# Kernel tuning notes

Measured on AMD Instinct MI355X. Metric: run time of the kernel, lower is better.

The kernel has to match this reference:

```python
import jax, jax.numpy as jnp
import numpy as np

D_MODEL = 1024
N_LAYER = 4
VOCAB = 50288  # 50277 padded to multiple of 16
D_STATE = 128
D_CONV = 4
HEADDIM = 64
CHUNK = 64
D_INNER = 2 * D_MODEL            # expand=2 -> 2048
NHEADS = D_INNER // HEADDIM      # 32
D_IN_PROJ = 2 * D_INNER + 2 * D_STATE + NHEADS  # ngroups=1
CONV_DIM = D_INNER + 2 * D_STATE
BATCH = 1
SEQLEN = 1024
EPS = 1e-5


def silu(x):
    return x * jax.nn.sigmoid(x)


def rmsnorm(x, w, z=None):
    if z is not None:
        x = x * silu(z)
    return x * jax.lax.rsqrt(jnp.mean(x * x, axis=-1, keepdims=True) + EPS) * w


def segsum(x):
    # x: (..., T) -> (..., T, T) with segment sums below diagonal, -inf above
    T = x.shape[-1]
    xe = jnp.broadcast_to(x[..., None], x.shape + (T,))
    mask_lo = jnp.tril(jnp.ones((T, T), dtype=bool), -1)
    xe = jnp.where(mask_lo, xe, 0.0)
    s = jnp.cumsum(xe, axis=-2)
    mask = jnp.tril(jnp.ones((T, T), dtype=bool), 0)
    return jnp.where(mask, s, -jnp.inf)


def ssd(x, dt, A, B, C, Dp):
    # x: (b,s,h,p), dt/A-broadcast: (b,s,h), B/C: (b,s,n) (ngroups=1), Dp: (h,)
    b, s = x.shape[0], x.shape[1]
    nchunks = s // CHUNK
    xD = x * Dp[:, None]
    Adt = A * dt                      # (b,s,h)
    xdt = x * dt[..., None]
    xr = xdt.reshape(b, nchunks, CHUNK, NHEADS, HEADDIM)
    Ar = Adt.reshape(b, nchunks, CHUNK, NHEADS).transpose(0, 3, 1, 2)  # (b,h,c,l)
    Br = B.reshape(b, nchunks, CHUNK, D_STATE)
    Cr = C.reshape(b, nchunks, CHUNK, D_STATE)
    A_cumsum = jnp.cumsum(Ar, axis=-1)                  # (b,h,c,l)
    L = jnp.exp(segsum(Ar))                             # (b,h,c,l,l)
    Y_diag = jnp.einsum('bcln,bcsn,bhcls,bcshp->bclhp', Cr, Br, L, xr)
    decay_states = jnp.exp(A_cumsum[..., -1:] - A_cumsum)
    states = jnp.einsum('bcln,bhcl,bclhp->bchpn', Br, decay_states, xr)
    states = jnp.concatenate([jnp.zeros_like(states[:, :1]), states], axis=1)
    decay_chunk = jnp.exp(segsum(jnp.pad(A_cumsum[..., -1], ((0, 0), (0, 0), (1, 0)))))
    new_states = jnp.einsum('bhzc,bchpn->bzhpn', decay_chunk, states)
    states = new_states[:, :-1]
    state_decay_out = jnp.exp(A_cumsum)
    Y_off = jnp.einsum('bcln,bchpn,bhcl->bclhp', Cr, states, state_decay_out)
    Y = (Y_diag + Y_off).reshape(b, s, NHEADS, HEADDIM) + xD
    return Y


def mamba2_forward(input_ids, embedding, norm_w, in_proj_w, conv_w, conv_b,
                   dt_bias, A_log, D, mixer_norm_w, out_proj_w, norm_f_w):
    h = embedding[input_ids]  # (b,s,d_model)
    for l in range(N_LAYER):
        u = rmsnorm(h, norm_w[l])
        zxbcdt = u @ in_proj_w[l].T  # (b,s,d_in_proj)
        z = zxbcdt[..., :D_INNER]
        xBC = zxbcdt[..., D_INNER:D_INNER + CONV_DIM]
        dt = jax.nn.softplus(zxbcdt[..., -NHEADS:] + dt_bias[l])
        # causal depthwise conv1d
        xc = jnp.transpose(xBC, (0, 2, 1))
        xc = jax.lax.conv_general_dilated(
            xc, conv_w[l], (1,), [(D_CONV - 1, 0)],
            dimension_numbers=('NCH', 'OIH', 'NCH'),
            feature_group_count=CONV_DIM) + conv_b[l][None, :, None]
        xBC = silu(jnp.transpose(xc, (0, 2, 1)))
        x = xBC[..., :D_INNER].reshape(BATCH, SEQLEN, NHEADS, HEADDIM)
        B = xBC[..., D_INNER:D_INNER + D_STATE]
        C = xBC[..., D_INNER + D_STATE:]
        A = -jnp.exp(A_log[l])  # (h,)
        y = ssd(x, dt, A, B, C, D[l])
        y = rmsnorm(y.reshape(BATCH, SEQLEN, D_INNER), mixer_norm_w[l], z)
        h = h + y @ out_proj_w[l].T
    h = rmsnorm(h, norm_f_w)
    return h @ embedding.T  # tied lm_head


def setup_inputs() -> dict:
    key = jax.random.key(0)
    ks = jax.random.split(key, 10)
    def rn(k, shape, s=0.02):
        return jax.random.normal(k, shape, jnp.float32) * s
    return {
        'input_ids': jax.random.randint(ks[0], (BATCH, SEQLEN), 0, VOCAB, jnp.int32),
        'embedding': rn(ks[1], (VOCAB, D_MODEL)),
        'norm_w': jnp.ones((N_LAYER, D_MODEL), jnp.float32),
        'in_proj_w': rn(ks[2], (N_LAYER, D_IN_PROJ, D_MODEL)),
        'conv_w': rn(ks[3], (N_LAYER, CONV_DIM, 1, D_CONV), 0.2),
        'conv_b': jnp.zeros((N_LAYER, CONV_DIM), jnp.float32),
        'dt_bias': rn(ks[4], (N_LAYER, NHEADS), 0.5),
        'A_log': jnp.log(jax.random.uniform(ks[5], (N_LAYER, NHEADS), jnp.float32, 1.0, 16.0)),
        'D': jnp.ones((N_LAYER, NHEADS), jnp.float32) + rn(ks[6], (N_LAYER, NHEADS), 0.1),
        'mixer_norm_w': jnp.ones((N_LAYER, D_INNER), jnp.float32),
        'out_proj_w': rn(ks[7], (N_LAYER, D_MODEL, D_INNER)),
        'norm_f_w': jnp.ones((D_MODEL,), jnp.float32),
    }


def reference(input_ids, embedding, norm_w, in_proj_w, conv_w, conv_b,
              dt_bias, A_log, D, mixer_norm_w, out_proj_w, norm_f_w):
    return mamba2_forward(input_ids, embedding, norm_w, in_proj_w, conv_w, conv_b,
                          dt_bias, A_log, D, mixer_norm_w, out_proj_w, norm_f_w)
```

## Files before the change

kernel.cpp:

```cpp
#include <hip/hip_runtime.h>
#include <hip/hip_bf16.h>
#include <math.h>

#define D_MODEL   1024
#define VOCAB     50288
#define D_STATE   128
#define D_CONV    4
#define HEADDIM   64
#define CHUNK     64
#define D_INNER   2048
#define NHEADS    32
#define D_IN_PROJ 4384
#define CONV_DIM  2304
#define SEQ       1024
#define NCHUNKS   16
#define EPS       1e-5f
#define SZH       1048576

typedef __bf16 bf16x8 __attribute__((ext_vector_type(8)));
typedef __bf16 bf16x4 __attribute__((ext_vector_type(4)));
typedef float  f32x4  __attribute__((ext_vector_type(4)));

__device__ __forceinline__ float blockReduceSum256(float v, float* sm) {
    #pragma unroll
    for (int off = 32; off > 0; off >>= 1) v += __shfl_down(v, off);
    if ((threadIdx.x & 63) == 0) sm[threadIdx.x >> 6] = v;
    __syncthreads();
    return sm[0] + sm[1] + sm[2] + sm[3];
}

__device__ __forceinline__ float sigmoidf_(float x) { return 1.0f / (1.0f + expf(-x)); }

__device__ __forceinline__ void gload_lds16(const __bf16* g, __bf16* l) {
    __builtin_amdgcn_global_load_lds(
        (const __attribute__((address_space(1))) void*)g,
        (__attribute__((address_space(3))) void*)l,
        16, 0, 0);
}

__global__ void cvt_bf16_k(const float* __restrict__ src, __bf16* __restrict__ dst, long n) {
    long i = ((long)blockIdx.x * 256 + threadIdx.x) * 8;
    long stride = (long)gridDim.x * 256 * 8;
    for (; i < n; i += stride) {
        float4 a = *(const float4*)(src + i);
        float4 b = *(const float4*)(src + i + 4);
        bf16x8 o;
        o[0] = (__bf16)a.x; o[1] = (__bf16)a.y; o[2] = (__bf16)a.z; o[3] = (__bf16)a.w;
        o[4] = (__bf16)b.x; o[5] = (__bf16)b.y; o[6] = (__bf16)b.z; o[7] = (__bf16)b.w;
        *(bf16x8*)(dst + i) = o;
    }
}

__global__ void gather_k(const int* __restrict__ ids, const float* __restrict__ emb,
                         float* __restrict__ h) {
    int s = blockIdx.x;
    int id = ids[s];
    const float4* src = (const float4*)(emb + (size_t)id * D_MODEL);
    float4* dst = (float4*)(h + (size_t)s * D_MODEL);
    dst[threadIdx.x] = src[threadIdx.x];
}

__global__ void rmsnorm_k(const float* __restrict__ x, const float* __restrict__ w,
                          float* __restrict__ o) {
    __shared__ float red[4];
    int s = blockIdx.x, t = threadIdx.x;
    float4 v = ((const float4*)(x + (size_t)s * D_MODEL))[t];
    float ss = v.x*v.x + v.y*v.y + v.z*v.z + v.w*v.w;
    float tot = blockReduceSum256(ss, red);
    float r = rsqrtf(tot / (float)D_MODEL + EPS);
    float4 wv = ((const float4*)w)[t];
    float4 ov;
    ov.x = v.x * r * wv.x; ov.y = v.y * r * wv.y;
    ov.z = v.z * r * wv.z; ov.w = v.w * r * wv.w;
    ((float4*)(o + (size_t)s * D_MODEL))[t] = ov;
}

__global__ void rmsnorm_fold_bf16_k(float* __restrict__ h, const float* __restrict__ o,
                                    const float* __restrict__ w, __bf16* __restrict__ out) {
    __shared__ float red[4];
    int s = blockIdx.x, t = threadIdx.x;
    float4 v = ((const float4*)(h + (size_t)s * D_MODEL))[t];
    if (o) {
        #pragma unroll
        for (int j = 0; j < 4; ++j) {
            float4 ov = ((const float4*)(o + (size_t)j * SZH + (size_t)s * D_MODEL))[t];
            v.x += ov.x; v.y += ov.y; v.z += ov.z; v.w += ov.w;
        }
        ((float4*)(h + (size_t)s * D_MODEL))[t] = v;
    }
    float ss = v.x*v.x + v.y*v.y + v.z*v.z + v.w*v.w;
    float tot = blockReduceSum256(ss, red);
    float r = rsqrtf(tot / (float)D_MODEL + EPS);
    float4 wv = ((const float4*)w)[t];
    bf16x4 ov;
    ov[0] = (__bf16)(v.x * r * wv.x); ov[1] = (__bf16)(v.y * r * wv.y);
    ov[2] = (__bf16)(v.z * r * wv.z); ov[3] = (__bf16)(v.w * r * wv.w);
    *(bf16x4*)(out + (size_t)s * D_MODEL + t * 4) = ov;
}

__global__ void gatednorm_k(float* __restrict__ Y, const float* __restrict__ zx,
                            const float* __restrict__ w) {
    __shared__ float red[4];
    int s = blockIdx.x, t = threadIdx.x;
    float4 y0 = ((const float4*)(Y + (size_t)s * D_INNER))[2*t];
    float4 y1 = ((const float4*)(Y + (size_t)s * D_INNER))[2*t+1];
    float4 z0 = ((const float4*)(zx + (size_t)s * D_IN_PROJ))[2*t];
    float4 z1 = ((const float4*)(zx + (size_t)s * D_IN_PROJ))[2*t+1];
    float g[8];
    float yv[8] = { y0.x,y0.y,y0.z,y0.w, y1.x,y1.y,y1.z,y1.w };
    float zv[8] = { z0.x,z0.y,z0.z,z0.w, z1.x,z1.y,z1.z,z1.w };
    float ss = 0.f;
    #pragma unroll
    for (int j = 0; j < 8; ++j) {
        float gg = yv[j] * zv[j] * sigmoidf_(zv[j]);
        g[j] = gg;
        ss += gg * gg;
    }
    float tot = blockReduceSum256(ss, red);
    float r = rsqrtf(tot / (float)D_INNER + EPS);
    float4 o0, o1;
    o0.x = g[0]*r*w[8*t+0]; o0.y = g[1]*r*w[8*t+1]; o0.z = g[2]*r*w[8*t+2]; o0.w = g[3]*r*w[8*t+3];
    o1.x = g[4]*r*w[8*t+4]; o1.y = g[5]*r*w[8*t+5]; o1.z = g[6]*r*w[8*t+6]; o1.w = g[7]*r*w[8*t+7];
    ((float4*)(Y + (size_t)s * D_INNER))[2*t]   = o0;
    ((float4*)(Y + (size_t)s * D_INNER))[2*t+1] = o1;
}

__global__ void gatednorm_bf16_k(const float* __restrict__ Y, const float* __restrict__ zx0,
                                 const float* __restrict__ zx1,
                                 const float* __restrict__ w, __bf16* __restrict__ o) {
    __shared__ float red[4];
    int s = blockIdx.x, t = threadIdx.x;
    float4 y0 = ((const float4*)(Y + (size_t)s * D_INNER))[2*t];
    float4 y1 = ((const float4*)(Y + (size_t)s * D_INNER))[2*t+1];
    float4 z0 = ((const float4*)(zx0 + (size_t)s * D_IN_PROJ))[2*t];
    float4 z1 = ((const float4*)(zx0 + (size_t)s * D_IN_PROJ))[2*t+1];
    if (zx1) {
        float4 a0 = ((const float4*)(zx1 + (size_t)s * D_IN_PROJ))[2*t];
        float4 a1 = ((const float4*)(zx1 + (size_t)s * D_IN_PROJ))[2*t+1];
        z0.x += a0.x; z0.y += a0.y; z0.z += a0.z; z0.w += a0.w;
        z1.x += a1.x; z1.y += a1.y; z1.z += a1.z; z1.w += a1.w;
    }
    float g[8];
    float yv[8] = { y0.x,y0.y,y0.z,y0.w, y1.x,y1.y,y1.z,y1.w };
    float zv[8] = { z0.x,z0.y,z0.z,z0.w, z1.x,z1.y,z1.z,z1.w };
    float ss = 0.f;
    #pragma unroll
    for (int j = 0; j < 8; ++j) {
        float gg = yv[j] * zv[j] * sigmoidf_(zv[j]);
        g[j] = gg;
        ss += gg * gg;
    }
    float tot = blockReduceSum256(ss, red);
    float r = rsqrtf(tot / (float)D_INNER + EPS);
    bf16x8 ov;
    #pragma unroll
    for (int j = 0; j < 8; ++j) ov[j] = (__bf16)(g[j] * r * w[8*t+j]);
    *(bf16x8*)(o + (size_t)s * D_INNER + t * 8) = ov;
}

template<int TM, int TN, int MTL2, bool ACC>
__global__ __launch_bounds__(256) void gemm_bt_bf16(const __bf16* __restrict__ A,
                                                    const __bf16* __restrict__ B,
                                                    float* __restrict__ C,
                                                    int N, int klen,
                                                    int lda, int ldb, int ldc,
                                                    int ntiles, size_t csplit) {
    constexpr int FM = TM / 32;
    constexpr int FN = TN / 32;
    __shared__ __bf16 As[TM * 32];
    __shared__ __bf16 Bs[TN * 32];

    const int d = blockIdx.x;
    const int xcd = d & 7;
    const int kk = d >> 3;
    const int p = kk >> MTL2;
    const int m_tile = kk & ((1 << MTL2) - 1);
    const int n_tile = xcd + (p << 3);
    if (n_tile >= ntiles) return;

    const int k_begin = blockIdx.y * klen;
    C += (size_t)blockIdx.y * csplit;

    const int bm0 = m_tile * TM;
    const int bn0 = n_tile * TN;
    const int t = threadIdx.x;
    const int l = t & 63;
    const int w = t >> 6;
    const int wr = w >> 1, wc = w & 1;
    const int lrow = l & 15;
    const int lk   = (l >> 4) * 8;
    const int srow = l >> 2;
    const int scol = (l & 3) * 8;

    f32x4 acc[FM][FN];
    #pragma unroll
    for (int m = 0; m < FM; ++m)
        #pragma unroll
        for (int n = 0; n < FN; ++n)
            acc[m][n] = (f32x4){0.f, 0.f, 0.f, 0.f};

    for (int k0 = k_begin; k0 < k_begin + klen; k0 += 32) {
        __syncthreads();
        #pragma unroll
        for (int i = 0; i < TM / 64; ++i) {
            int r0 = w * (TM / 4) + i * 16;
            const __bf16* g = A + (size_t)(bm0 + r0 + srow) * lda + k0 + scol;
            gload_lds16(g, As + (size_t)r0 * 32);
        }
        #pragma unroll
        for (int i = 0; i < TN / 64; ++i) {
            int r0 = w * (TN / 4) + i * 16;
            int gn = bn0 + r0 + srow; if (gn > N - 1) gn = N - 1;
            const __bf16* g = B + (size_t)gn * ldb + k0 + scol;
            gload_lds16(g, Bs + (size_t)r0 * 32);
        }
        __syncthreads();

        bf16x8 af[FM], bfr[FN];
        #pragma unroll
        for (int m = 0; m < FM; ++m)
            af[m] = *(const bf16x8*)&As[(wr * (TM/2) + m * 16 + lrow) * 32 + lk];
        #pragma unroll
        for (int n = 0; n < FN; ++n)
            bfr[n] = *(const bf16x8*)&Bs[(wc * (TN/2) + n * 16 + lrow) * 32 + lk];
        #pragma unroll
        for (int m = 0; m < FM; ++m)
            #pragma unroll
            for (int n = 0; n < FN; ++n)
                acc[m][n] = __builtin_amdgcn_mfma_f32_16x16x32_bf16(af[m], bfr[n], acc[m][n], 0, 0, 0);
    }

    const int r0 = (l >> 4) * 4;
    #pragma unroll
    for (int m = 0; m < FM; ++m) {
        #pragma unroll
        for (int rr = 0; rr < 4; ++rr) {
            int gr = bm0 + wr * (TM/2) + m * 16 + r0 + rr;
            #pragma unroll
            for (int n = 0; n < FN; ++n) {
                int gc = bn0 + wc * (TN/2) + n * 16 + lrow;
                if (gc < N) {
                    size_t off = (size_t)gr * ldc + gc;
                    if (ACC) C[off] += acc[m][n][rr];
                    else     C[off]  = acc[m][n][rr];
                }
            }
        }
    }
}

template<bool ACC>
__global__ __launch_bounds__(256) void gemm_nt_cvt(const float* __restrict__ A,
                                                   const float* __restrict__ B,
                                                   float* __restrict__ C,
                                                   int M, int N, int K,
                                                   int lda, int ldb, int ldc) {
    __shared__ __bf16 As[128][40];
    __shared__ __bf16 Bs[128][40];
    const int bm0 = blockIdx.x * 128;
    const int bn0 = blockIdx.y * 128;
    const int t = threadIdx.x;
    const int l = t & 63;
    const int w = t >> 6;
    const int wr = w >> 1;
    const int wc = w & 1;
    const int lrow = l & 15;
    const int lk   = (l >> 4) * 8;

    f32x4 acc[4][4];
    #pragma unroll
    for (int m = 0; m < 4; ++m)
        #pragma unroll
        for (int n = 0; n < 4; ++n)
            acc[m][n] = (f32x4){0.f, 0.f, 0.f, 0.f};

    for (int k0 = 0; k0 < K; k0 += 32) {
        __syncthreads();
        float4 av[4], bv[4];
        #pragma unroll
        for (int i = 0; i < 4; ++i) {
            int idx = t + i * 256;
            int r = idx >> 3;
            int c4 = (idx & 7) * 4;
            av[i] = *(const float4*)(A + (size_t)(bm0 + r) * lda + k0 + c4);
            int gn = bn0 + r; if (gn > N - 1) gn = N - 1;
            bv[i] = *(const float4*)(B + (size_t)gn * ldb + k0 + c4);
        }
        #pragma unroll
        for (int i = 0; i < 4; ++i) {
            int idx = t + i * 256;
            int r = idx >> 3;
            int c4 = (idx & 7) * 4;
            bf16x4 aw, bw;
            aw[0] = (__bf16)av[i].x; aw[1] = (__bf16)av[i].y;
            aw[2] = (__bf16)av[i].z; aw[3] = (__bf16)av[i].w;
            bw[0] = (__bf16)bv[i].x; bw[1] = (__bf16)bv[i].y;
            bw[2] = (__bf16)bv[i].z; bw[3] = (__bf16)bv[i].w;
            *(bf16x4*)&As[r][c4] = aw;
            *(bf16x4*)&Bs[r][c4] = bw;
        }
        __syncthreads();

        bf16x8 af[4], bfr[4];
        #pragma unroll
        for (int m = 0; m < 4; ++m)
            af[m] = *(const bf16x8*)&As[wr * 64 + m * 16 + lrow][lk];
        #pragma unroll
        for (int n = 0; n < 4; ++n)
            bfr[n] = *(const bf16x8*)&Bs[wc * 64 + n * 16 + lrow][lk];
        #pragma unroll
        for (int m = 0; m < 4; ++m)
            #pragma unroll
            for (int n = 0; n < 4; ++n)
                acc[m][n] = __builtin_amdgcn_mfma_f32_16x16x32_bf16(af[m], bfr[n], acc[m][n], 0, 0, 0);
    }

    const int r0 = (l >> 4) * 4;
    #pragma unroll
    for (int m = 0; m < 4; ++m) {
        #pragma unroll
        for (int rr = 0; rr < 4; ++rr) {
            int gr = bm0 + wr * 64 + m * 16 + r0 + rr;
            #pragma unroll
            for (int n = 0; n < 4; ++n) {
                int gc = bn0 + wc * 64 + n * 16 + lrow;
                if (gc < N) {
                    size_t off = (size_t)gr * ldc + gc;
                    if (ACC) C[off] += acc[m][n][rr];
                    else     C[off]  = acc[m][n][rr];
                }
            }
        }
    }
}

__global__ void conv_silu_k(const float* __restrict__ zx0, const float* __restrict__ zx1,
                            const float* __restrict__ w,
                            const float* __restrict__ b, float* __restrict__ xBC) {
    int idx = blockIdx.x * 256 + threadIdx.x;
    if (idx >= SEQ * CONV_DIM) return;
    int s = idx / CONV_DIM, c = idx - s * CONV_DIM;
    float acc = b[c];
    #pragma unroll
    for (int k = 0; k < D_CONV; ++k) {
        int si = s + k - (D_CONV - 1);
        if (si >= 0) {
            size_t o = (size_t)si * D_IN_PROJ + D_INNER + c;
            float v = zx0[o];
            if (zx1) v += zx1[o];
            acc = fmaf(v, w[c * D_CONV + k], acc);
        }
    }
    xBC[idx] = acc * sigmoidf_(acc);
}

__global__ void dtcum_k(const float* __restrict__ zx0, const float* __restrict__ zx1,
                        const float* __restrict__ dt_bias,
                        const float* __restrict__ A_log,
                        float* __restrict__ dtb, float* __restrict__ acs) {
    int c = blockIdx.x, h = blockIdx.y, l = threadIdx.x;
    int s = c * 64 + l;
    size_t o = (size_t)s * D_IN_PROJ + (D_IN_PROJ - NHEADS) + h;
    float v = zx0[o];
    if (zx1) v += zx1[o];
    v += dt_bias[h];
    float dt = (v > 20.f) ? v : log1pf(expf(v));
    dtb[(size_t)s * NHEADS + h] = dt;
    float a = -expf(A_log[h]);
    float x = a * dt;
    #pragma unroll
    for (int off = 1; off < 64; off <<= 1) {
        float oo = __shfl_up(x, off);
        if (l >= off) x += oo;
    }
    acs[(size_t)h * SEQ + s] = x;
}

__global__ __launch_bounds__(256) void cmg_k(const float* __restrict__ xBC,
                                             float* __restrict__ cm,
                                             __bf16* __restrict__ btg) {
    const int c = blockIdx.x;
    const int LDP = 136;
    __shared__ __bf16 Cs[64 * 136];
    __shared__ __bf16 Bs[64 * 136];
    const int t = threadIdx.x;
    const int l = t & 63;
    const int w = t >> 6;

    #pragma unroll
    for (int i = 0; i < 8; ++i) {
        int e = t + i * 256;
        int row = e >> 5, n4 = (e & 31) * 4;
        float4 vc = *(const float4*)(xBC + (size_t)(c*64 + row) * CONV_DIM + D_INNER + D_STATE + n4);
        float4 vb = *(const float4*)(xBC + (size_t)(c*64 + row) * CONV_DIM + D_INNER + n4);
        bf16x4 cc, bb;
        cc[0] = (__bf16)vc.x; cc[1] = (__bf16)vc.y; cc[2] = (__bf16)vc.z; cc[3] = (__bf16)vc.w;
        bb[0] = (__bf16)vb.x; bb[1] = (__bf16)vb.y; bb[2] = (__bf16)vb.z; bb[3] = (__bf16)vb.w;
        *(bf16x4*)&Cs[row * LDP + n4] = cc;
        *(bf16x4*)&Bs[row * LDP + n4] = bb;
    }
    __syncthreads();

    #pragma unroll
    for (int i = 0; i < 4; ++i) {
        int e8 = t + i * 256;
        int n = e8 >> 3, l8 = (e8 & 7) * 8;
        bf16x8 o;
        #pragma unroll
        for (int j = 0; j < 8; ++j) o[j] = Bs[(l8 + j) * LDP + n];
        *(bf16x8*)(btg + ((size_t)c * 128 + n) * 64 + l8) = o;
    }

    const int lrow = l & 15;
    const int lk   = (l >> 4) * 8;
    const int l0 = w * 16;
    f32x4 acc[4];
    #pragma unroll
    for (int n = 0; n < 4; ++n) acc[n] = (f32x4){0.f,0.f,0.f,0.f};
    #pragma unroll
    for (int kc = 0; kc < 4; ++kc) {
        bf16x8 a = *(const bf16x8*)&Cs[(l0 + lrow) * LDP + kc * 32 + lk];
        #pragma unroll
        for (int n = 0; n < 4; ++n) {
            bf16x8 b = *(const bf16x8*)&Bs[(n * 16 + lrow) * LDP + kc * 32 + lk];
            acc[n] = __builtin_amdgcn_mfma_f32_16x16x32_bf16(a, b, acc[n], 0, 0, 0);
        }
    }
    const int r0 = (l >> 4) * 4;
    #pragma unroll
    for (int n = 0; n < 4; ++n)
        #pragma unroll
        for (int r = 0; r < 4; ++r)
            cm[(size_t)c * 4096 + (l0 + r0 + r) * 64 + n * 16 + lrow] = acc[n][r];
}

__global__ __launch_bounds__(256) void ydst_k(const float* __restrict__ cm,
                                              const __bf16* __restrict__ btg,
                                              const float* __restrict__ xBC,
                                              const float* __restrict__ dtb,
                                              const float* __restrict__ acs,
                                              float* __restrict__ Y,
                                              float* __restrict__ st) {
    const int c = blockIdx.x, h = blockIdx.y;
    const int LDP = 72;
    __shared__ __bf16 Xt[64 * 72];
    __shared__ __bf16 X2[64 * 72];
    __shared__ __bf16 G [64 * 72];
    __shared__ __bf16 Bt[128 * 72];
    __shared__ float arow[64];
    __shared__ float decl[64];
    const int t = threadIdx.x;
    const int l = t & 63;
    const int w = t >> 6;

    if (t < 64) arow[t] = acs[(size_t)h * SEQ + c * 64 + t];
    __syncthreads();
    const float alast = arow[63];
    if (t < 64) decl[t] = expf(alast - arow[t]);
    #pragma unroll
    for (int i = 0; i < 16; ++i) {
        int e = t + i * 256;
        int gl = e >> 6, sx = e & 63;
        G[gl * LDP + sx] = (sx <= gl) ? (__bf16)(cm[(size_t)c * 4096 + e] * expf(arow[gl] - arow[sx])) : (__bf16)0.f;
    }
    #pragma unroll
    for (int i = 0; i < 4; ++i) {
        int e8 = t + i * 256;
        int n = e8 >> 3, l8 = (e8 & 7) * 8;
        *(bf16x8*)&Bt[n * LDP + l8] = *(const bf16x8*)(btg + ((size_t)c * 128 + n) * 64 + l8);
    }
    __syncthreads();
    #pragma unroll
    for (int i = 0; i < 4; ++i) {
        int e4 = t + i * 256;
        int sx = e4 >> 4, p4 = (e4 & 15) * 4;
        int s = c * 64 + sx;
        float4 v = *(const float4*)(xBC + (size_t)s * CONV_DIM + h * HEADDIM + p4);
        float d = dtb[(size_t)s * NHEADS + h];
        float d2 = d * decl[sx];
        Xt[(p4+0) * LDP + sx] = (__bf16)(v.x * d);
        Xt[(p4+1) * LDP + sx] = (__bf16)(v.y * d);
        Xt[(p4+2) * LDP + sx] = (__bf16)(v.z * d);
        Xt[(p4+3) * LDP + sx] = (__bf16)(v.w * d);
        X2[(p4+0) * LDP + sx] = (__bf16)(v.x * d2);
        X2[(p4+1) * LDP + sx] = (__bf16)(v.y * d2);
        X2[(p4+2) * LDP + sx] = (__bf16)(v.z * d2);
        X2[(p4+3) * LDP + sx] = (__bf16)(v.w * d2);
    }
    __syncthreads();

    const int lrow = l & 15;
    const int lk   = (l >> 4) * 8;
    const int p0 = w * 16;
    const int r0 = (l >> 4) * 4;

    f32x4 acc1[4];
    #pragma unroll
    for (int n = 0; n < 4; ++n) acc1[n] = (f32x4){0.f,0.f,0.f,0.f};
    #pragma unroll
    for (int kc = 0; kc < 2; ++kc) {
        bf16x8 a = *(const bf16x8*)&Xt[(p0 + lrow) * LDP + kc * 32 + lk];
        #pragma unroll
        for (int n = 0; n < 4; ++n) {
            bf16x8 b = *(const bf16x8*)&G[(n * 16 + lrow) * LDP + kc * 32 + lk];
            acc1[n] = __builtin_amdgcn_mfma_f32_16x16x32_bf16(a, b, acc1[n], 0, 0, 0);
        }
    }
    #pragma unroll
    for (int n = 0; n < 4; ++n) {
        int lc = n * 16 + lrow;
        float4 ov; ov.x = acc1[n][0]; ov.y = acc1[n][1]; ov.z = acc1[n][2]; ov.w = acc1[n][3];
        *(float4*)(Y + (size_t)(c*64 + lc) * D_INNER + h * HEADDIM + p0 + r0) = ov;
    }

    f32x4 acc2[8];
    #pragma unroll
    for (int n = 0; n < 8; ++n) acc2[n] = (f32x4){0.f,0.f,0.f,0.f};
    #pragma unroll
    for (int kc = 0; kc < 2; ++kc) {
        bf16x8 a = *(const bf16x8*)&X2[(p0 + lrow) * LDP + kc * 32 + lk];
        #pragma unroll
        for (int n = 0; n < 8; ++n) {
            bf16x8 b = *(const bf16x8*)&Bt[(n * 16 + lrow) * LDP + kc * 32 + lk];
            acc2[n] = __builtin_amdgcn_mfma_f32_16x16x32_bf16(a, b, acc2[n], 0, 0, 0);
        }
    }
    float* stb = st + ((size_t)(c * NHEADS + h) * 64) * 128;
    #pragma unroll
    for (int n = 0; n < 8; ++n) {
        int nc = n * 16 + lrow;
        #pragma unroll
        for (int r = 0; r < 4; ++r)
            stb[(size_t)(p0 + r0 + r) * 128 + nc] = acc2[n][r];
    }
}

__global__ void rec_k(float* __restrict__ st, const float* __restrict__ acs) {
    int idx = blockIdx.x * 256 + threadIdx.x;
    int h = idx >> 13;
    float S = 0.f;
    for (int c = 0; c < NCHUNKS; ++c) {
        float* p = st + (size_t)c * (NHEADS * D_STATE * HEADDIM) + idx;
        float tmp = *p;
        *p = S;
        float dec = expf(acs[(size_t)h * SEQ + c * 64 + 63]);
        S = fmaf(S, dec, tmp);
    }
}

__global__ __launch_bounds__(256) void yoff_k(const float* __restrict__ xBC,
                                              const float* __restrict__ acs,
                                              const float* __restrict__ st,
                                              const float* __restrict__ Dp,
                                              float* __restrict__ Y) {
    const int c = blockIdx.x, h = blockIdx.y;
    const int LDP = 136;
    __shared__ __bf16 Sts[64 * 136];
    __shared__ __bf16 Cs [64 * 136];
    __shared__ float arow[64];
    const int t = threadIdx.x;
    const int l = t & 63;
    const int w = t >> 6;

    if (t < 64) arow[t] = acs[(size_t)h * SEQ + c * 64 + t];
    const float* stb = st + ((size_t)(c * NHEADS + h) * 64) * 128;
    #pragma unroll
    for (int i = 0; i < 8; ++i) {
        int e = t + i * 256;
        int row = e >> 5, n4 = (e & 31) * 4;
        float4 vs = *(const float4*)(stb + (size_t)row * 128 + n4);
        float4 vc = *(const float4*)(xBC + (size_t)(c*64 + row) * CONV_DIM + D_INNER + D_STATE + n4);
        bf16x4 ss, cc;
        ss[0] = (__bf16)vs.x; ss[1] = (__bf16)vs.y; ss[2] = (__bf16)vs.z; ss[3] = (__bf16)vs.w;
        cc[0] = (__bf16)vc.x; cc[1] = (__bf16)vc.y; cc[2] = (__bf16)vc.z; cc[3] = (__bf16)vc.w;
        *(bf16x4*)&Sts[row * LDP + n4] = ss;
        *(bf16x4*)&Cs [row * LDP + n4] = cc;
    }
    __syncthreads();

    const int lrow = l & 15;
    const int lk   = (l >> 4) * 8;
    const int p0 = w * 16;
    const int r0 = (l >> 4) * 4;
    const float dpar = Dp[h];

    f32x4 acc[4];
    #pragma unroll
    for (int n = 0; n < 4; ++n) acc[n] = (f32x4){0.f,0.f,0.f,0.f};
    #pragma unroll
    for (int kc = 0; kc < 4; ++kc) {
        bf16x8 a = *(const bf16x8*)&Sts[(p0 + lrow) * LDP + kc * 32 + lk];
        #pragma unroll
        for (int n = 0; n < 4; ++n) {
            bf16x8 b = *(const bf16x8*)&Cs[(n * 16 + lrow) * LDP + kc * 32 + lk];
            acc[n] = __builtin_amdgcn_mfma_f32_16x16x32_bf16(a, b, acc[n], 0, 0, 0);
        }
    }
    #pragma unroll
    for (int n = 0; n < 4; ++n) {
        int lc = n * 16 + lrow;
        int s = c * 64 + lc;
        float sc = expf(arow[lc]);
        float4 xv = *(const float4*)(xBC + (size_t)s * CONV_DIM + h * HEADDIM + p0 + r0);
        float4 yv = *(float4*)(Y + (size_t)s * D_INNER + h * HEADDIM + p0 + r0);
        yv.x += sc * acc[n][0] + dpar * xv.x;
        yv.y += sc * acc[n][1] + dpar * xv.y;
        yv.z += sc * acc[n][2] + dpar * xv.z;
        yv.w += sc * acc[n][3] + dpar * xv.w;
        *(float4*)(Y + (size_t)s * D_INNER + h * HEADDIM + p0 + r0) = yv;
    }
}

extern "C" void kernel_launch(void* const* d_in, const int* in_sizes, int n_in,
                              void* d_out, int out_size, void* d_ws, size_t ws_size,
                              hipStream_t stream) {
    const int*   ids          = (const int*)d_in[0];
    const float* emb          = (const float*)d_in[1];
    const float* norm_w       = (const float*)d_in[2];
    const float* in_proj_w    = (const float*)d_in[3];
    const float* conv_w       = (const float*)d_in[4];
    const float* conv_b       = (const float*)d_in[5];
    const float* dt_bias      = (const float*)d_in[6];
    const float* A_log        = (const float*)d_in[7];
    const float* Dp           = (const float*)d_in[8];
    const float* mixer_norm_w = (const float*)d_in[9];
    const float* out_proj_w   = (const float*)d_in[10];
    const float* norm_f_w     = (const float*)d_in[11];
    float* out = (float*)d_out;

    const size_t SZ_H = SZH, SZ_U = SZH, SZ_ZX = 4489216, SZ_XBC = 2359296,
                 SZ_DT = 32768, SZ_ACS = 32768, SZ_CM = 65536, SZ_ST = 4194304, SZ_Y = 2097152;
    const size_t SZ_BTG_F = 65536;
    const size_t BF_U = SZ_H, BF_Y = SZ_Y;
    const size_t BF_WIN  = 4ull * 4489216;
    const size_t BF_WOUT = 4ull * 2097152;
    const size_t BF_EMB  = (size_t)VOCAB * D_MODEL;

    const size_t f32_base = SZ_H + SZ_U + SZ_ZX + SZ_XBC + SZ_DT + SZ_ACS + SZ_CM + SZ_BTG_F + SZ_ST + SZ_Y;
    const size_t f32_new  = f32_base + SZ_ZX + 4 * SZ_H;
    const size_t bf_all   = (BF_U + BF_Y + BF_WIN + BF_WOUT + BF_EMB) * 2;
    const size_t bytesNew = f32_new * 4 + bf_all;
    const size_t bytesOld = f32_base * 4 + bf_all;
    const int tier = (ws_size >= bytesNew) ? 0 : (ws_size >= bytesOld) ? 1 : 2;

    float *h, *u, *dtb, *acs, *cm, *zx, *zxb = nullptr, *xBC, *st, *Y, *o = nullptr;
    __bf16 *btg, *ub = nullptr, *Yb = nullptr, *win = nullptr, *wout = nullptr, *embb = nullptr;

    if (tier <= 1) {
        float* f = (float*)d_ws;
        h = f;   f += SZ_H;
        u = f;   f += SZ_U;
        dtb = f; f += SZ_DT;
        acs = f; f += SZ_ACS;
        cm = f;  f += SZ_CM;
        btg = (__bf16*)f; f += SZ_BTG_F;
        zx = f;  f += SZ_ZX;
        if (tier == 0) {
            zxb = f; f += SZ_ZX;
            o = f;   f += 4 * SZ_H;
        }
        xBC = f; f += SZ_XBC;
        st = f;  f += SZ_ST;
        Y = f;   f += SZ_Y;
        __bf16* bb = (__bf16*)f;
        ub = bb;   bb += BF_U;
        Yb = bb;   bb += BF_Y;
        win = bb;  bb += BF_WIN;
        wout = bb; bb += BF_WOUT;
        embb = bb;
    } else {
        float* f = (float*)d_ws;
        h = f;   f += SZ_H;
        u = f;   f += SZ_U;
        dtb = f; f += SZ_DT;
        acs = f; f += SZ_ACS;
        cm = f;  f += SZ_CM;
        btg = (__bf16*)f; f += SZ_BTG_F;
        float* ob = (float*)d_out;
        zx = ob;
        xBC = zx + SZ_ZX;
        st = xBC + SZ_XBC;
        Y = st + SZ_ST;
    }

    if (tier <= 1) {
        cvt_bf16_k<<<(int)(BF_WIN / 2048), 256, 0, stream>>>(in_proj_w, win, (long)BF_WIN);
        cvt_bf16_k<<<(int)(BF_WOUT / 2048), 256, 0, stream>>>(out_proj_w, wout, (long)BF_WOUT);
        cvt_bf16_k<<<(int)(BF_EMB / 2048), 256, 0, stream>>>(emb, embb, (long)BF_EMB);
    }

    gather_k<<<SEQ, 256, 0, stream>>>(ids, emb, h);

    const int NT_IN  = (D_IN_PROJ + 127) / 128;
    const int NT_OUT = D_MODEL / 128;
    const int NT_LM  = (VOCAB + 127) / 128;
    const int GX_IN  = 8 * ((NT_IN  + 7) / 8) * 8;
    const int GX_OUT = 8 * ((NT_OUT + 7) / 8) * 16;
    const int GX_LM  = 8 * ((NT_LM  + 7) / 8) * 8;

    for (int l = 0; l < 4; ++l) {
        if (tier <= 1) {
            rmsnorm_fold_bf16_k<<<SEQ, 256, 0, stream>>>(
                h, (tier == 0 && l > 0) ? o : nullptr, norm_w + (size_t)l * D_MODEL, ub);
            if (tier == 0) {
                gemm_bt_bf16<128, 128, 3, false><<<dim3(GX_IN, 2), 256, 0, stream>>>(
                    ub, win + (size_t)l * 4489216, zx,
                    D_IN_PROJ, 512, D_MODEL, D_MODEL, D_IN_PROJ, NT_IN, SZ_ZX);
            } else {
                gemm_bt_bf16<128, 128, 3, false><<<dim3(GX_IN, 1), 256, 0, stream>>>(
                    ub, win + (size_t)l * 4489216, zx,
                    D_IN_PROJ, 1024, D_MODEL, D_MODEL, D_IN_PROJ, NT_IN, 0);
            }
        } else {
            rmsnorm_k<<<SEQ, 256, 0, stream>>>(h, norm_w + (size_t)l * D_MODEL, u);
            gemm_nt_cvt<false><<<dim3(8, 35), 256, 0, stream>>>(
                u, in_proj_w + (size_t)l * D_IN_PROJ * D_MODEL, zx,
                SEQ, D_IN_PROJ, D_MODEL, D_MODEL, D_MODEL, D_IN_PROJ);
        }

        float* zx1 = (tier == 0) ? zxb : nullptr;

        conv_silu_k<<<(SEQ * CONV_DIM) / 256, 256, 0, stream>>>(
            zx, zx1, conv_w + (size_t)l * CONV_DIM * D_CONV, conv_b + (size_t)l * CONV_DIM, xBC);

        dtcum_k<<<dim3(NCHUNKS, NHEADS), 64, 0, stream>>>(
            zx, zx1, dt_bias + (size_t)l * NHEADS, A_log + (size_t)l * NHEADS, dtb, acs);

        cmg_k<<<NCHUNKS, 256, 0, stream>>>(xBC, cm, btg);

        ydst_k<<<dim3(NCHUNKS, NHEADS), 256, 0, stream>>>(cm, btg, xBC, dtb, acs, Y, st);

        rec_k<<<(NHEADS * D_STATE * HEADDIM) / 256, 256, 0, stream>>>(st, acs);

        yoff_k<<<dim3(NCHUNKS, NHEADS), 256, 0, stream>>>(xBC, acs, st, Dp + (size_t)l * NHEADS, Y);

        if (tier <= 1) {
            gatednorm_bf16_k<<<SEQ, 256, 0, stream>>>(Y, zx, zx1, mixer_norm_w + (size_t)l * D_INNER, Yb);
            if (tier == 0) {
                gemm_bt_bf16<64, 128, 4, false><<<dim3(GX_OUT, 4), 256, 0, stream>>>(
                    Yb, wout + (size_t)l * 2097152, o,
                    D_MODEL, 512, D_INNER, D_INNER, D_MODEL, NT_OUT, SZ_H);
            } else {
                gemm_bt_bf16<64, 128, 4, true><<<dim3(GX_OUT, 1), 256, 0, stream>>>(
                    Yb, wout + (size_t)l * 2097152, h,
                    D_MODEL, 2048, D_INNER, D_INNER, D_MODEL, NT_OUT, 0);
            }
        } else {
            gatednorm_k<<<SEQ, 256, 0, stream>>>(Y, zx, mixer_norm_w + (size_t)l * D_INNER);
            gemm_nt_cvt<true><<<dim3(8, 8), 256, 0, stream>>>(
                Y, out_proj_w + (size_t)l * D_MODEL * D_INNER, h,
                SEQ, D_MODEL, D_INNER, D_INNER, D_INNER, D_MODEL);
        }
    }

    if (tier <= 1) {
        rmsnorm_fold_bf16_k<<<SEQ, 256, 0, stream>>>(
            h, (tier == 0) ? o : nullptr, norm_f_w, ub);
        gemm_bt_bf16<128, 128, 3, false><<<dim3(GX_LM, 1), 256, 0, stream>>>(
            ub, embb, out, VOCAB, 1024, D_MODEL, D_MODEL, VOCAB, NT_LM, 0);
    } else {
        rmsnorm_k<<<SEQ, 256, 0, stream>>>(h, norm_f_w, u);
        gemm_nt_cvt<false><<<dim3(8, (VOCAB + 127) / 128), 256, 0, stream>>>(
            u, emb, out, SEQ, VOCAB, D_MODEL, D_MODEL, D_MODEL, VOCAB);
    }
}
```

Measured before the change: 721.5 us.

## Use 256x256-tile 512-thread double-buffered GEMM for the LM head

```diff
diff --git a/kernel.cpp b/kernel.cpp
--- a/kernel.cpp
+++ b/kernel.cpp
@@ -156,6 +156,116 @@
     #pragma unroll
     for (int j = 0; j < 8; ++j) ov[j] = (__bf16)(g[j] * r * w[8*t+j]);
     *(bf16x8*)(o + (size_t)s * D_INNER + t * 8) = ov;
+}
+
+__global__ __launch_bounds__(512) void gemm256_8ph(const __bf16* __restrict__ A,
+                                                   const __bf16* __restrict__ B,
+                                                   float* __restrict__ C,
+                                                   int N, int K,
+                                                   int lda, int ldb, int ldc,
+                                                   int ntiles) {
+    extern __shared__ __bf16 lds[];
+
+    const int d = blockIdx.x;
+    const int xcd = d & 7, kk = d >> 3;
+    const int m_tile = kk & 3, p = kk >> 2;
+    const int n_tile = xcd + (p << 3);
+    if (n_tile >= ntiles) return;
+    const int bm0 = m_tile * 256, bn0 = n_tile * 256;
+
+    const int tid = threadIdx.x;
+    const int l = tid & 63, w = tid >> 6;
+    const int wr = w >> 2, wc = w & 3;
+    const int lrow = l & 15;
+    const int kb8 = (((l >> 4) ^ ((l >> 1) & 3)) << 3);
+    const int srow_off = (w << 4) + (l >> 2);
+    const int sk8 = (((l & 3) ^ ((l >> 3) & 3)) << 3);
+
+    f32x4 acc[8][4];
+    #pragma unroll
+    for (int m = 0; m < 8; ++m)
+        #pragma unroll
+        for (int n = 0; n < 4; ++n) acc[m][n] = (f32x4){0.f,0.f,0.f,0.f};
+
+    auto stage = [&](int kt, int b) {
+        __bf16* base = lds + b * 16384;
+        #pragma unroll
+        for (int r = 0; r < 2; ++r) {
+            int row = r * 128 + srow_off;
+            const __bf16* g = A + (size_t)(bm0 + row) * lda + kt * 32 + sk8;
+            gload_lds16(g, base + r * 4096 + w * 512);
+        }
+        #pragma unroll
+        for (int r = 0; r < 2; ++r) {
+            int row = r * 128 + srow_off;
+            int grn = bn0 + row; if (grn > N - 1) grn = N - 1;
+            const __bf16* g = B + (size_t)grn * ldb + kt * 32 + sk8;
+            gload_lds16(g, base + 8192 + r * 4096 + w * 512);
+        }
+    };
+
+    stage(0, 0);
+    stage(1, 1);
+    asm volatile("s_waitcnt vmcnt(4)" ::: "memory");
+    __builtin_amdgcn_s_barrier();
+
+    const int nt = K / 32;
+    for (int t = 0; t < nt; ++t) {
+        const int b = t & 1;
+        const int bb = b * 16384;
+        bf16x8 af[4], bfv[4];
+        #pragma unroll
+        for (int m = 0; m < 4; ++m)
+            af[m] = *(const bf16x8*)&lds[bb + (wr * 128 + m * 16 + lrow) * 32 + kb8];
+        #pragma unroll
+        for (int n = 0; n < 4; ++n)
+            bfv[n] = *(const bf16x8*)&lds[bb + 8192 + (wc * 64 + n * 16 + lrow) * 32 + kb8];
+        __builtin_amdgcn_s_barrier();
+        __builtin_amdgcn_s_setprio(1);
+        #pragma unroll
+        for (int m = 0; m < 4; ++m)
+            #pragma unroll
+            for (int n = 0; n < 4; ++n)
+                acc[m][n] = __builtin_amdgcn_mfma_f32_16x16x32_bf16(af[m], bfv[n], acc[m][n], 0, 0, 0);
+        __builtin_amdgcn_s_setprio(0);
+        __builtin_amdgcn_s_barrier();
+        #pragma unroll
+        for (int m = 0; m < 4; ++m)
+            af[m] = *(const bf16x8*)&lds[bb + (wr * 128 + (m + 4) * 16 + lrow) * 32 + kb8];
+        __builtin_amdgcn_s_barrier();
+        __builtin_amdgcn_s_setprio(1);
+        #pragma unroll
+        for (int m = 0; m < 4; ++m)
+            #pragma unroll
+            for (int n = 0; n < 4; ++n)
+                acc[m + 4][n] = __builtin_amdgcn_mfma_f32_16x16x32_bf16(af[m], bfv[n], acc[m + 4][n], 0, 0, 0);
+        __builtin_amdgcn_s_setprio(0);
+        __builtin_amdgcn_s_barrier();
+        asm volatile("" ::: "memory");
+        if (t + 2 < nt) {
+            stage(t + 2, b);
+            asm volatile("s_waitcnt vmcnt(4)" ::: "memory");
+            __builtin_amdgcn_s_barrier();
+        } else if (t + 1 < nt) {
+            asm volatile("s_waitcnt vmcnt(0)" ::: "memory");
+            __builtin_amdgcn_s_barrier();
+        }
+    }
+
+    const int r0q = (l >> 4) * 4;
+    #pragma unroll
+    for (int m = 0; m < 8; ++m) {
+        int gr = bm0 + wr * 128 + m * 16 + r0q;
+        #pragma unroll
+        for (int n = 0; n < 4; ++n) {
+            int gc = bn0 + wc * 64 + n * 16 + lrow;
+            if (gc < N) {
+                #pragma unroll
+                for (int rr = 0; rr < 4; ++rr)
+                    C[(size_t)(gr + rr) * ldc + gc] = acc[m][n][rr];
+            }
+        }
+    }
 }
 
 template<int TM, int TN, int MTL2, bool ACC>
@@ -693,10 +803,10 @@
 
     const int NT_IN  = (D_IN_PROJ + 127) / 128;
     const int NT_OUT = D_MODEL / 128;
-    const int NT_LM  = (VOCAB + 127) / 128;
     const int GX_IN  = 8 * ((NT_IN  + 7) / 8) * 8;
     const int GX_OUT = 8 * ((NT_OUT + 7) / 8) * 16;
-    const int GX_LM  = 8 * ((NT_LM  + 7) / 8) * 8;
+    const int NT_LM256 = (VOCAB + 255) / 256;
+    const int GX_LM256 = 8 * ((NT_LM256 + 7) / 8) * 4;
 
     for (int l = 0; l < 4; ++l) {
         if (tier <= 1) {
@@ -756,8 +866,8 @@
     if (tier <= 1) {
         rmsnorm_fold_bf16_k<<<SEQ, 256, 0, stream>>>(
             h, (tier == 0) ? o : nullptr, norm_f_w, ub);
-        gemm_bt_bf16<128, 128, 3, false><<<dim3(GX_LM, 1), 256, 0, stream>>>(
-            ub, embb, out, VOCAB, 1024, D_MODEL, D_MODEL, VOCAB, NT_LM, 0);
+        gemm256_8ph<<<dim3(GX_LM256), 512, 65536, stream>>>(
+            ub, embb, out, VOCAB, 1024, D_MODEL, D_MODEL, VOCAB, NT_LM256);
     } else {
         rmsnorm_k<<<SEQ, 256, 0, stream>>>(h, norm_f_w, u);
         gemm_nt_cvt<false><<<dim3(8, (VOCAB + 127) / 128), 256, 0, stream>>>(
```

New measurement: 720.3 us. About the same (-0.2%).
